# Performance work log

Hardware: AMD Instinct MI355X
Metric: run time of the kernel (lower is better)

The kernel has to match this reference:

```python
import jax, jax.numpy as jnp
import numpy as np

NEG_POS_RATIO = 3
B, P, C = 128, 8732, 21  # batch, SSD300 priors, VOC classes (hardcoded 21 in original)


def setup_inputs() -> dict:
    key = jax.random.key(0)
    k1, k2, k3, k4, k5, k6 = jax.random.split(key, 6)
    confidence = jax.random.normal(k1, (B, P, C), jnp.float32)
    predicted_locations = jax.random.normal(k2, (B, P, 4), jnp.float32)
    gt_locations = jax.random.normal(k3, (B, P, 4), jnp.float32)
    raw_labels = jax.random.randint(k4, (B, P), 0, C)
    keep = jax.random.uniform(k5, (B, P)) < 0.03
    labels = jnp.where(keep, raw_labels, 0).astype(jnp.int64)
    mask = jax.random.uniform(k6, (B, P), jnp.float32)
    return {
        "confidence": confidence,
        "predicted_locations": predicted_locations,
        "labels": labels,
        "gt_locations": gt_locations,
        "mask": mask,
    }


def _hard_negative_mining(bg_loss, labels, neg_pos_ratio):
    # Faithful to SSD box_utils.hard_negative_mining.
    pos_mask = labels > 0                                   # [B,P] bool
    num_pos = pos_mask.sum(axis=1, keepdims=True)           # [B,1]
    num_neg = num_pos * neg_pos_ratio                       # [B,1]
    masked = jnp.where(pos_mask, -jnp.inf, bg_loss)         # positives excluded
    idx = jnp.argsort(-masked, axis=1)                      # descending by loss
    orders = jnp.argsort(idx, axis=1)                       # rank of each prior
    neg_mask = orders < num_neg                             # top num_neg hardest
    return pos_mask, neg_mask


def reference(confidence, predicted_locations, labels, gt_locations, mask):
    nls = -jax.nn.log_softmax(confidence, axis=-1)          # [B,P,C]
    bg_loss = nls[:, :, 0]                                  # [B,P]
    pos_mask, neg_mask = _hard_negative_mining(bg_loss, labels, NEG_POS_RATIO)
    posf = pos_mask.astype(nls.dtype)

    # per-prior NLL at the assigned label, weighted by mask over positives
    per_label = jnp.take_along_axis(nls, labels[..., None], axis=2)[..., 0]  # [B,P]
    confidence_pos_loss = (mask * per_label * posf).sum()
    confidence_neg_loss = jnp.where(neg_mask, bg_loss, 0.0).sum()
    confidence_loss = confidence_pos_loss + confidence_neg_loss

    # smooth-L1 over positive priors, weighted by mask (broadcast over 4 coords)
    d = predicted_locations - gt_locations                  # [B,P,4]
    ad = jnp.abs(d)
    sl1 = jnp.where(ad < 1.0, 0.5 * d * d, ad - 0.5)
    regression_loss = (sl1 * (mask * posf)[..., None]).sum()

    all_batch_pos = mask.sum()
    return regression_loss / all_batch_pos, confidence_loss / all_batch_pos
```

## Files before the change

### kernel.cpp

```cpp
#include <hip/hip_runtime.h>
#include <stdint.h>

#define BATCH  128
#define PRI    8732
#define NCLS   21
#define NPR    3
#define TOTAL  (BATCH * PRI)
#define CPW    2
#define NWAVE  (TOTAL / (64 * CPW))
#define GBLK   (NWAVE / 4)


__global__ __launch_bounds__(256, 1)
void k_main(const float* __restrict__ conf, const float* __restrict__ pred,
            const int* __restrict__ labels, const float* __restrict__ gt,
            const float* __restrict__ mask, uint32_t* __restrict__ keys,
            float* __restrict__ pm, float* __restrict__ pp, float* __restrict__ pr)
{
  __shared__ __align__(16) float scratch[4 * 64 * NCLS];
  const int tid = threadIdx.x;
  const int wv  = tid >> 6;
  const int ln  = tid & 63;
  const int gw  = blockIdx.x * 4 + wv;

  float*  sl  = scratch + wv * (64 * NCLS);
  float4* sl4 = (float4*)sl;
  const long long base0 = (long long)gw * (64 * CPW);

  float4 q[CPW][5], qt[CPW], pd[CPW], g[CPW];
  int    lab[CPW];
  float  mk[CPW];
  #pragma unroll
  for (int c = 0; c < CPW; ++c) {
    const long long c0 = base0 + (long long)c * 64;
    const float4* s4 = (const float4*)(conf + c0 * NCLS);
    #pragma unroll
    for (int j = 0; j < 5; ++j) q[c][j] = s4[j * 64 + ln];
    if (ln < 16) qt[c] = s4[320 + ln];
    lab[c] = labels[c0 + ln];
    mk[c]  = mask  [c0 + ln];
    pd[c]  = ((const float4*)pred)[c0 + ln];
    g[c]   = ((const float4*)gt)[c0 + ln];
  }

  float accm = 0.f, accp = 0.f, accr = 0.f;

  #pragma unroll
  for (int c = 0; c < CPW; ++c) {
    const long long a = base0 + (long long)c * 64 + ln;

    __builtin_amdgcn_wave_barrier();
    #pragma unroll
    for (int j = 0; j < 5; ++j) sl4[j * 64 + ln] = q[c][j];
    if (ln < 16) sl4[320 + ln] = qt[c];
    __builtin_amdgcn_wave_barrier();

    const float* cp = sl + ln * NCLS;
    float cv[NCLS];
    #pragma unroll
    for (int i = 0; i < NCLS; ++i) cv[i] = cp[i];

    float m = cv[0];
    #pragma unroll
    for (int i = 1; i < NCLS; ++i) m = fmaxf(m, cv[i]);
    float s = 0.f, selv = cv[0];
    #pragma unroll
    for (int i = 0; i < NCLS; ++i) {
      s += __expf(cv[i] - m);
      if (i > 0) selv = (lab[c] == i) ? cv[i] : selv;
    }
    const float lse = m + __logf(s);
    const float bg  = lse - cv[0];
    const bool  pos = lab[c] > 0;

    float slr = 0.f, d, ad;
    d = pd[c].x - g[c].x; ad = fabsf(d); slr += (ad < 1.f) ? 0.5f * d * d : ad - 0.5f;
    d = pd[c].y - g[c].y; ad = fabsf(d); slr += (ad < 1.f) ? 0.5f * d * d : ad - 0.5f;
    d = pd[c].z - g[c].z; ad = fabsf(d); slr += (ad < 1.f) ? 0.5f * d * d : ad - 0.5f;
    d = pd[c].w - g[c].w; ad = fabsf(d); slr += (ad < 1.f) ? 0.5f * d * d : ad - 0.5f;
    const float w = pos ? mk[c] : 0.f;
    accm += mk[c];
    accp += w * (lse - selv);
    accr += w * slr;

    keys[a] = pos ? 0u : (__float_as_uint(bg) | 0x80000000u);
  }

  #pragma unroll
  for (int o = 32; o > 0; o >>= 1) {
    accm += __shfl_down(accm, o);
    accp += __shfl_down(accp, o);
    accr += __shfl_down(accr, o);
  }
  if (ln == 0) { pm[gw] = accm; pp[gw] = accp; pr[gw] = accr; }
}

#define SEL_T 512
#define RPT   18

__global__ __launch_bounds__(SEL_T)
void k_select(const uint32_t* __restrict__ keys, double* __restrict__ neg)
{
  __shared__ int    slots[16 * 24 + 8];
  __shared__ int    ired[8];
  __shared__ double dred[8];
  const int tid  = threadIdx.x;
  const int w    = tid >> 6;
  const int lane = tid & 63;
  const uint32_t* row = keys + (size_t)blockIdx.x * PRI;

  uint32_t kr[RPT];
  #pragma unroll
  for (int r = 0; r < 17; ++r) kr[r] = row[tid + 512 * r];
  kr[17] = (tid < 28) ? row[tid + 8704] : 0u;

  int zc = 0;
  #pragma unroll
  for (int r = 0; r < 17; ++r) zc += (kr[r] == 0u) ? 1 : 0;
  if (tid < 28) zc += (kr[17] == 0u) ? 1 : 0;
  #pragma unroll
  for (int o = 32; o > 0; o >>= 1) zc += __shfl_down(zc, o);
  if (lane == 0) ired[w] = zc;
  __syncthreads();
  int np = 0;
  #pragma unroll
  for (int i = 0; i < 8; ++i) np += ired[i];

  int k = np * NPR;
  const int nneg = PRI - np;
  if (k > nneg) k = nneg;

  double result = 0.0;
  if (k > 0) {
    uint32_t cur = 0x80000000u;
    #pragma unroll 1
    for (int bit = 30; bit >= 1; bit -= 2) {
      const int rnd = (30 - bit) >> 1;
      const uint32_t tA = cur | (3u << (bit - 1));
      const uint32_t tB = cur | (1u << bit);
      const uint32_t tC = cur | (1u << (bit - 1));
      int cA = 0, cB = 0, cC = 0;
      #pragma unroll
      for (int r = 0; r < RPT; ++r) {
        cA += (int)__popcll(__ballot(kr[r] >= tA));
        cB += (int)__popcll(__ballot(kr[r] >= tB));
        cC += (int)__popcll(__ballot(kr[r] >= tC));
      }
      if (lane == 0) {
        int* sl = &slots[rnd * 24];
        sl[w] = cA; sl[8 + w] = cB; sl[16 + w] = cC;
      }
      __syncthreads();
      int TA = 0, TB = 0, TC = 0;
      const int* sl = &slots[rnd * 24];
      #pragma unroll
      for (int i = 0; i < 8; ++i) { TA += sl[i]; TB += sl[8 + i]; TC += sl[16 + i]; }
      cur = (TA >= k) ? tA : (TB >= k) ? tB : (TC >= k) ? tC : cur;
    }
    {
      const uint32_t t = cur | 1u;
      int c = 0;
      #pragma unroll
      for (int r = 0; r < RPT; ++r) c += (int)__popcll(__ballot(kr[r] >= t));
      if (lane == 0) slots[16 * 24 + w] = c;
      __syncthreads();
      int tot = 0;
      #pragma unroll
      for (int i = 0; i < 8; ++i) tot += slots[16 * 24 + i];
      if (tot >= k) cur = t;
    }

    const float thr = __uint_as_float(cur & 0x7fffffffu);
    double ssum = 0.0;
    int g = 0;
    #pragma unroll
    for (int r = 0; r < RPT; ++r) {
      if (kr[r] > cur) { ssum += (double)__uint_as_float(kr[r] & 0x7fffffffu); ++g; }
    }
    #pragma unroll
    for (int o = 32; o > 0; o >>= 1) { ssum += __shfl_down(ssum, o); g += __shfl_down(g, o); }
    if (lane == 0) { dred[w] = ssum; ired[w] = g; }
    __syncthreads();
    if (tid == 0) {
      double tot = 0.0; int gg = 0;
      #pragma unroll
      for (int i = 0; i < 8; ++i) { tot += dred[i]; gg += ired[i]; }
      result = tot + (double)(k - gg) * (double)thr;
    }
  }
  if (tid == 0) neg[blockIdx.x] = result;
}

__global__ __launch_bounds__(256)
void k_final(const float* __restrict__ pm, const float* __restrict__ pp,
             const float* __restrict__ pr, const double* __restrict__ neg,
             float* __restrict__ out)
{
  __shared__ double red[4][4];
  const int tid = threadIdx.x, w = tid >> 6, lane = tid & 63;
  double sm = 0.0, sp = 0.0, sr = 0.0, sn = 0.0;
  for (int i = tid; i < NWAVE; i += 256) {
    sm += (double)pm[i]; sp += (double)pp[i]; sr += (double)pr[i];
  }
  if (tid < BATCH) sn = neg[tid];
  #pragma unroll
  for (int o = 32; o > 0; o >>= 1) {
    sm += __shfl_down(sm, o); sp += __shfl_down(sp, o);
    sr += __shfl_down(sr, o); sn += __shfl_down(sn, o);
  }
  if (lane == 0) { red[0][w] = sm; red[1][w] = sp; red[2][w] = sr; red[3][w] = sn; }
  __syncthreads();
  if (tid == 0) {
    double m = 0, p = 0, r = 0, n = 0;
    #pragma unroll
    for (int i = 0; i < 4; ++i) { m += red[0][i]; p += red[1][i]; r += red[2][i]; n += red[3][i]; }
    out[0] = (float)(r / m);
    out[1] = (float)((p + n) / m);
  }
}

extern "C" void kernel_launch(void* const* d_in, const int* in_sizes, int n_in,
                              void* d_out, int out_size, void* d_ws, size_t ws_size,
                              hipStream_t stream) {
  const float* conf   = (const float*)d_in[0];
  const float* pred   = (const float*)d_in[1];
  const int*   labels = (const int*)d_in[2];
  const float* gt     = (const float*)d_in[3];
  const float* mask   = (const float*)d_in[4];
  float* out = (float*)d_out;

  char* ws = (char*)d_ws;
  const size_t keys_bytes = (size_t)TOTAL * sizeof(uint32_t);
  uint32_t* keys = (uint32_t*)ws;
  float*  pm  = (float*)(ws + keys_bytes);
  float*  pp  = pm + NWAVE;
  float*  pr  = pp + NWAVE;
  double* neg = (double*)(ws + keys_bytes +
                          (((size_t)3 * NWAVE * sizeof(float) + 7) & ~(size_t)7));

  k_main<<<GBLK, 256, 0, stream>>>(conf, pred, labels, gt, mask, keys, pm, pp, pr);
  k_select<<<BATCH, SEL_T, 0, stream>>>(keys, neg);
  k_final<<<1, 256, 0, stream>>>(pm, pp, pr, neg, out);
}
```

Baseline: 217.3 us.

## Double-buffer confidence tiles via direct global-to-LDS loads and skip loc loads for negatives

Confidence rows are now streamed straight into LDS with global_load_lds into a double buffer, four 64-prior chunks per wave. Hand-placed s_waitcnt counters overlap the next chunk's load with the current chunk's softmax. Pred/gt locations are now loaded only for positive priors, removing most of that traffic, and the occupancy hint of one block per SM is dropped. The manual vmcnt accounting is fragile: if the compiler issues a different number of outstanding memory ops, a chunk could be read from LDS before it has arrived. The grid also now has a ragged last block, handled by an early return.

```diff
diff --git a/kernel.cpp b/kernel.cpp
--- a/kernel.cpp
+++ b/kernel.cpp
@@ -6,85 +6,108 @@
 #define NCLS   21
 #define NPR    3
 #define TOTAL  (BATCH * PRI)
-#define CPW    2
+#define CPW    4
 #define NWAVE  (TOTAL / (64 * CPW))
-#define GBLK   (NWAVE / 4)
-
-
-__global__ __launch_bounds__(256, 1)
+#define GBLK   ((NWAVE + 3) / 4)
+
+
+typedef const __attribute__((address_space(1))) void gv_t;
+typedef __attribute__((address_space(3))) void lv_t;
+
+__device__ __forceinline__ void dma_chunk(const float* __restrict__ conf,
+                                          float* dst, long long c0, int ln) {
+  const float*  src = conf + c0 * NCLS;
+  const float4* s4  = (const float4*)src;
+  float4*       d4  = (float4*)dst;
+  #pragma unroll
+  for (int j = 0; j < 5; ++j)
+    __builtin_amdgcn_global_load_lds((gv_t*)(s4 + j * 64 + ln),
+                                     (lv_t*)(d4 + j * 64), 16, 0, 0);
+  __builtin_amdgcn_global_load_lds((gv_t*)(src + 1280 + ln),
+                                   (lv_t*)(dst + 1280), 4, 0, 0);
+}
+
+__device__ __forceinline__ void do_chunk(const float* sl, int ln, long long a,
+                                         int lab, float mk,
+                                         const float4* __restrict__ pred4,
+                                         const float4* __restrict__ gt4,
+                                         uint32_t* __restrict__ keys,
+                                         float& accm, float& accp, float& accr)
+{
+  const float* cp = sl + ln * NCLS;
+  float cv[NCLS];
+  #pragma unroll
+  for (int i = 0; i < NCLS; ++i) cv[i] = cp[i];
+  float m = cv[0];
+  #pragma unroll
+  for (int i = 1; i < NCLS; ++i) m = fmaxf(m, cv[i]);
+  float s = 0.f, selv = cv[0];
+  #pragma unroll
+  for (int i = 0; i < NCLS; ++i) {
+    s += __expf(cv[i] - m);
+    if (i > 0) selv = (lab == i) ? cv[i] : selv;
+  }
+  const float lse = m + __logf(s);
+  const float bg  = lse - cv[0];
+  const bool  pos = lab > 0;
+  accm += mk;
+  if (pos) {
+    accp += mk * (lse - selv);
+    const float4 pd = pred4[a];
+    const float4 g  = gt4[a];
+    float sl1 = 0.f, d, ad;
+    d = pd.x - g.x; ad = fabsf(d); sl1 += (ad < 1.f) ? 0.5f * d * d : ad - 0.5f;
+    d = pd.y - g.y; ad = fabsf(d); sl1 += (ad < 1.f) ? 0.5f * d * d : ad - 0.5f;
+    d = pd.z - g.z; ad = fabsf(d); sl1 += (ad < 1.f) ? 0.5f * d * d : ad - 0.5f;
+    d = pd.w - g.w; ad = fabsf(d); sl1 += (ad < 1.f) ? 0.5f * d * d : ad - 0.5f;
+    accr += mk * sl1;
+  }
+  keys[a] = pos ? 0u : (__float_as_uint(bg) | 0x80000000u);
+}
+
+__global__ __launch_bounds__(256)
 void k_main(const float* __restrict__ conf, const float* __restrict__ pred,
             const int* __restrict__ labels, const float* __restrict__ gt,
             const float* __restrict__ mask, uint32_t* __restrict__ keys,
             float* __restrict__ pm, float* __restrict__ pp, float* __restrict__ pr)
 {
-  __shared__ __align__(16) float scratch[4 * 64 * NCLS];
+  __shared__ __align__(16) float scratch[2][4][64 * NCLS];
   const int tid = threadIdx.x;
   const int wv  = tid >> 6;
   const int ln  = tid & 63;
   const int gw  = blockIdx.x * 4 + wv;
-
-  float*  sl  = scratch + wv * (64 * NCLS);
-  float4* sl4 = (float4*)sl;
-  const long long base0 = (long long)gw * (64 * CPW);
-
-  float4 q[CPW][5], qt[CPW], pd[CPW], g[CPW];
-  int    lab[CPW];
-  float  mk[CPW];
-  #pragma unroll
-  for (int c = 0; c < CPW; ++c) {
-    const long long c0 = base0 + (long long)c * 64;
-    const float4* s4 = (const float4*)(conf + c0 * NCLS);
-    #pragma unroll
-    for (int j = 0; j < 5; ++j) q[c][j] = s4[j * 64 + ln];
-    if (ln < 16) qt[c] = s4[320 + ln];
-    lab[c] = labels[c0 + ln];
-    mk[c]  = mask  [c0 + ln];
-    pd[c]  = ((const float4*)pred)[c0 + ln];
-    g[c]   = ((const float4*)gt)[c0 + ln];
-  }
+  if (gw >= NWAVE) return;
+
+  const long long b0 = (long long)gw * (64 * CPW);
+  const float4* pred4 = (const float4*)pred;
+  const float4* gt4   = (const float4*)gt;
+  float* buf0 = &scratch[0][wv][0];
+  float* buf1 = &scratch[1][wv][0];
+
+  dma_chunk(conf, buf0, b0, ln);
+  int lab0 = labels[b0 + ln];        float mk0 = mask[b0 + ln];
+  dma_chunk(conf, buf1, b0 + 64, ln);
+  int lab1 = labels[b0 + 64 + ln];   float mk1 = mask[b0 + 64 + ln];
 
   float accm = 0.f, accp = 0.f, accr = 0.f;
 
-  #pragma unroll
-  for (int c = 0; c < CPW; ++c) {
-    const long long a = base0 + (long long)c * 64 + ln;
-
-    __builtin_amdgcn_wave_barrier();
-    #pragma unroll
-    for (int j = 0; j < 5; ++j) sl4[j * 64 + ln] = q[c][j];
-    if (ln < 16) sl4[320 + ln] = qt[c];
-    __builtin_amdgcn_wave_barrier();
-
-    const float* cp = sl + ln * NCLS;
-    float cv[NCLS];
-    #pragma unroll
-    for (int i = 0; i < NCLS; ++i) cv[i] = cp[i];
-
-    float m = cv[0];
-    #pragma unroll
-    for (int i = 1; i < NCLS; ++i) m = fmaxf(m, cv[i]);
-    float s = 0.f, selv = cv[0];
-    #pragma unroll
-    for (int i = 0; i < NCLS; ++i) {
-      s += __expf(cv[i] - m);
-      if (i > 0) selv = (lab[c] == i) ? cv[i] : selv;
-    }
-    const float lse = m + __logf(s);
-    const float bg  = lse - cv[0];
-    const bool  pos = lab[c] > 0;
-
-    float slr = 0.f, d, ad;
-    d = pd[c].x - g[c].x; ad = fabsf(d); slr += (ad < 1.f) ? 0.5f * d * d : ad - 0.5f;
-    d = pd[c].y - g[c].y; ad = fabsf(d); slr += (ad < 1.f) ? 0.5f * d * d : ad - 0.5f;
-    d = pd[c].z - g[c].z; ad = fabsf(d); slr += (ad < 1.f) ? 0.5f * d * d : ad - 0.5f;
-    d = pd[c].w - g[c].w; ad = fabsf(d); slr += (ad < 1.f) ? 0.5f * d * d : ad - 0.5f;
-    const float w = pos ? mk[c] : 0.f;
-    accm += mk[c];
-    accp += w * (lse - selv);
-    accr += w * slr;
-
-    keys[a] = pos ? 0u : (__float_as_uint(bg) | 0x80000000u);
-  }
+  asm volatile("s_waitcnt vmcnt(8)" ::: "memory");
+  do_chunk(buf0, ln, b0 + ln, lab0, mk0, pred4, gt4, keys, accm, accp, accr);
+  asm volatile("s_waitcnt lgkmcnt(0)" ::: "memory");
+  dma_chunk(conf, buf0, b0 + 128, ln);
+  int lab2 = labels[b0 + 128 + ln];  float mk2 = mask[b0 + 128 + ln];
+
+  asm volatile("s_waitcnt vmcnt(8)" ::: "memory");
+  do_chunk(buf1, ln, b0 + 64 + ln, lab1, mk1, pred4, gt4, keys, accm, accp, accr);
+  asm volatile("s_waitcnt lgkmcnt(0)" ::: "memory");
+  dma_chunk(conf, buf1, b0 + 192, ln);
+  int lab3 = labels[b0 + 192 + ln];  float mk3 = mask[b0 + 192 + ln];
+
+  asm volatile("s_waitcnt vmcnt(8)" ::: "memory");
+  do_chunk(buf0, ln, b0 + 128 + ln, lab2, mk2, pred4, gt4, keys, accm, accp, accr);
+
+  asm volatile("s_waitcnt vmcnt(0)" ::: "memory");
+  do_chunk(buf1, ln, b0 + 192 + ln, lab3, mk3, pred4, gt4, keys, accm, accp, accr);
 
   #pragma unroll
   for (int o = 32; o > 0; o >>= 1) {
```

After: 198.0 us. 1.1x faster.
